# Kernel optimization log

Measured on AMD Instinct MI355X. Metric: run time of the kernel, lower is better.

Reference implementation:

```python
import jax, jax.numpy as jnp
from jax import lax
import numpy as np

B, H, W, D_MODEL = 2, 64, 64, 192
D_INNER, D_STATE, DT_RANK = 384, 16, 12
L = H * W
LN_EPS = 1e-5


def setup_inputs() -> dict:
    ks = jax.random.split(jax.random.key(0), 12)
    rng = np.random.default_rng(0)
    perm = rng.permutation(L).astype(np.int32)

    def p(i, shape, scale=0.02):
        return jax.random.normal(ks[i], shape, dtype=jnp.float32) * scale

    return {
        "x": jax.random.normal(ks[0], (B, H, W, D_MODEL), dtype=jnp.float32),
        "condition": jax.random.normal(ks[1], (B, H, W, D_MODEL), dtype=jnp.float32),
        "W_in": p(2, (2 * D_INNER, D_MODEL)),
        "W_con": p(3, (D_INNER, D_MODEL)),
        "conv_w": p(4, (D_INNER, 1, 3, 3)),
        "conv_b": jnp.zeros((D_INNER,), jnp.float32),
        "con_conv_w": p(5, (D_INNER, 1, 3, 3)),
        "con_conv_b": jnp.zeros((D_INNER,), jnp.float32),
        "x_proj_w": p(6, (DT_RANK + 2 * D_STATE, D_INNER)),
        "dt_proj_w": p(7, (D_INNER, DT_RANK)),
        "dt_proj_b": p(8, (D_INNER,), 0.1),
        "A_logs": jnp.tile(jnp.log(jnp.arange(1, D_STATE + 1, dtype=jnp.float32))[None, :], (D_INNER, 1)),
        "Ds": jnp.ones((D_INNER,), jnp.float32),
        "ln_w": jnp.ones((D_INNER,), jnp.float32),
        "ln_b": jnp.zeros((D_INNER,), jnp.float32),
        "W_out": p(9, (D_MODEL, D_INNER)),
        "scan_path": jnp.asarray(perm),
        "rev_scan_path": jnp.asarray(np.argsort(perm).astype(np.int32)),
    }


def _dwconv(x, w, b):
    # depthwise 3x3 conv, SAME padding; x: [B, C, H, W], w: [C, 1, 3, 3]
    y = lax.conv_general_dilated(x, w, (1, 1), "SAME",
                                 dimension_numbers=("NCHW", "OIHW", "NCHW"),
                                 feature_group_count=x.shape[1])
    return y + b[None, :, None, None]


def _selective_scan(u, delta, A, Bs, Cs, D):
    # u, delta: [B, D, L]; A: [D, N]; Bs, Cs: [B, N, L]; D: [D]
    dA = jnp.exp(jnp.einsum("bdl,dn->lbdn", delta, A))          # [L, B, D, N]
    dBu = jnp.einsum("bdl,bnl,bdl->lbdn", delta, Bs, u)          # [L, B, D, N]
    Ct = jnp.transpose(Cs, (2, 0, 1))                             # [L, B, N]
    h0 = jnp.zeros(dA.shape[1:], dA.dtype)

    def step(h, inp):
        a, b, c = inp
        h = a * h + b
        return h, jnp.einsum("bdn,bn->bd", h, c)

    _, ys = lax.scan(step, h0, (dA, dBu, Ct))                     # ys: [L, B, D]
    y = jnp.transpose(ys, (1, 2, 0))                              # [B, D, L]
    return y + u * D[None, :, None]


def _forward(x, condition, W_in, W_con, conv_w, conv_b, con_conv_w, con_conv_b,
             x_proj_w, dt_proj_w, dt_proj_b, A_logs, Ds, ln_w, ln_b, W_out,
             scan_path, rev_scan_path):
    b, h, w, _ = x.shape
    l = h * w
    xz = x @ W_in.T                                               # [B, H, W, 2*Din]
    xa, z = jnp.split(xz, 2, axis=-1)
    z = jax.nn.silu(z)
    c = condition @ W_con.T
    xa = jax.nn.silu(_dwconv(jnp.transpose(xa, (0, 3, 1, 2)), conv_w, conv_b))
    c = jax.nn.silu(_dwconv(jnp.transpose(c, (0, 3, 1, 2)), con_conv_w, con_conv_b))
    d = xa.shape[1]
    xs = xa.reshape(b, d, l)[:, :, scan_path]                     # forward_permutation, K=1
    cs = c.reshape(b, d, l)[:, :, scan_path]
    x_dbl = jnp.einsum("bdl,cd->bcl", xs + cs, x_proj_w)          # [B, R+2N, L]
    r, n = dt_proj_w.shape[1], A_logs.shape[1]
    dts = jnp.einsum("brl,dr->bdl", x_dbl[:, :r], dt_proj_w)
    Bs = x_dbl[:, r:r + n]
    Cs = x_dbl[:, r + n:]
    A = -jnp.exp(A_logs)
    delta = jax.nn.softplus(dts + dt_proj_b[None, :, None])       # delta_softplus=True
    y = _selective_scan(xs, delta, A, Bs, Cs, Ds)                 # [B, D, L]
    y = y[:, :, rev_scan_path]                                    # backward_permutation
    y = jnp.transpose(y, (0, 2, 1))                               # [B, L, D]
    mu = jnp.mean(y, axis=-1, keepdims=True)
    var = jnp.var(y, axis=-1, keepdims=True)
    y = (y - mu) * lax.rsqrt(var + LN_EPS) * ln_w + ln_b          # out_norm
    y = y.reshape(b, h, w, d) * z
    return y @ W_out.T                                            # out_proj (no bias)


def reference(x, condition, W_in, W_con, conv_w, conv_b, con_conv_w, con_conv_b,
              x_proj_w, dt_proj_w, dt_proj_b, A_logs, Ds, ln_w, ln_b, W_out,
              scan_path, rev_scan_path):
    return _forward(x, condition, W_in, W_con, conv_w, conv_b, con_conv_w,
                    con_conv_b, x_proj_w, dt_proj_w, dt_proj_b, A_logs, Ds,
                    ln_w, ln_b, W_out, scan_path, rev_scan_path)
```

## Files before the change

### kernel.cpp

```cpp
#include <hip/hip_runtime.h>
#include <math.h>

#define BB 2
#define HH 64
#define WW 64
#define DM 192
#define DI 384
#define NS 16
#define DTR 12
#define LL 4096
#define ROWS (BB*LL)
#define NCHUNK 64
#define LCHUNK 64
#define NCOMB 448

typedef __attribute__((ext_vector_type(8))) short bf16x8;
typedef __attribute__((ext_vector_type(4))) float f32x4;

__device__ __forceinline__ float silu_f(float v) {
    return v / (1.0f + __expf(-v));
}

__device__ __forceinline__ unsigned short f2bf(float f) {
    union { float f; unsigned int u; } c; c.f = f;
    unsigned int u = c.u;
    u += 0x7fffu + ((u >> 16) & 1u);
    return (unsigned short)(u >> 16);
}

__global__ __launch_bounds__(256) void cast_bf16(
    const float* __restrict__ in, unsigned short* __restrict__ out, int n4)
{
    int i = blockIdx.x * 256 + threadIdx.x;
    if (i >= n4) return;
    float4 v = ((const float4*)in)[i];
    ushort4 o;
    o.x = f2bf(v.x); o.y = f2bf(v.y); o.z = f2bf(v.z); o.w = f2bf(v.w);
    ((ushort4*)out)[i] = o;
}

__global__ __launch_bounds__(256) void cast_weights(
    const float* __restrict__ w_in, const float* __restrict__ w_con,
    const float* __restrict__ w_out,
    unsigned short* __restrict__ w_in_bf, unsigned short* __restrict__ w_con_bf,
    unsigned short* __restrict__ w_out_bf)
{
    int i = blockIdx.x * 256 + threadIdx.x;
    if (i >= 73728) return;
    const float4* src; ushort4* dst; int off;
    if (i < 36864)      { src = (const float4*)w_in;  dst = (ushort4*)w_in_bf;  off = i; }
    else if (i < 55296) { src = (const float4*)w_con; dst = (ushort4*)w_con_bf; off = i - 36864; }
    else                { src = (const float4*)w_out; dst = (ushort4*)w_out_bf; off = i - 55296; }
    float4 v = src[off];
    ushort4 o;
    o.x = f2bf(v.x); o.y = f2bf(v.y); o.z = f2bf(v.z); o.w = f2bf(v.w);
    dst[off] = o;
}

__global__ __launch_bounds__(256) void make_wcomb(
    const float* __restrict__ x_proj_w,
    const float* __restrict__ dt_w,
    unsigned short* __restrict__ wc)
{
    int idx = blockIdx.x * 256 + threadIdx.x;
    if (idx >= NCOMB * DI) return;
    int row = idx / DI, k = idx - row * DI;
    float v = 0.f;
    if (row < 384) {
        const float* dw = dt_w + row * DTR;
        #pragma unroll
        for (int r = 0; r < DTR; ++r) v += dw[r] * x_proj_w[r * DI + k];
    } else if (row < 416) {
        v = x_proj_w[(12 + (row - 384)) * DI + k];
    }
    wc[idx] = f2bf(v);
}

__device__ __forceinline__ void gemm_epilogue(
    int mode, int row, int col, int N, float v,
    const float* __restrict__ bias,
    float* __restrict__ out0, float* __restrict__ out1)
{
    if (mode == 0) {
        if (col < 384) out0[(size_t)row * 384 + col] = v;
        else           out1[(size_t)row * 384 + (col - 384)] = silu_f(v);
    } else if (mode == 1) {
        out0[(size_t)row * N + col] = v;
    } else {
        if (col < 384) {
            float a = v + bias[col];
            out0[(size_t)row * 384 + col] = (a > 20.f) ? a : log1pf(__expf(a));
        } else if (col < 416) {
            int idx = col - 384;
            int pos = (idx < 16) ? ((idx & 7) * 4 + (idx >> 3))
                                 : (((idx - 16) & 7) * 4 + 2 + ((idx - 16) >> 3));
            out1[(size_t)row * 32 + pos] = v;
        }
    }
}

__global__ __launch_bounds__(256) void gemm_bf16(
    const unsigned short* __restrict__ A, const unsigned short* __restrict__ W,
    const float* __restrict__ bias,
    float* __restrict__ out0, float* __restrict__ out1,
    int M, int N, int K, int mode)
{
    __shared__ __align__(16) unsigned short sA[64 * 40];
    __shared__ __align__(16) unsigned short sB[64 * 40];
    const int bm = blockIdx.x * 64;
    const int bn = blockIdx.y * 64;
    const int tid  = threadIdx.x;
    const int wave = tid >> 6;
    const int lane = tid & 63;
    const int quad = lane >> 4;
    const int l16  = lane & 15;

    const int lrow = tid >> 2;
    const int lkof = (tid & 3) * 8;

    f32x4 acc[4];
    #pragma unroll
    for (int t = 0; t < 4; ++t) acc[t] = (f32x4)(0.f);

    const int arow = (wave * 16 + l16) * 40 + quad * 8;

    for (int k0 = 0; k0 < K; k0 += 32) {
        *(bf16x8*)&sA[lrow * 40 + lkof] =
            *(const bf16x8*)&A[(size_t)(bm + lrow) * K + k0 + lkof];
        *(bf16x8*)&sB[lrow * 40 + lkof] =
            *(const bf16x8*)&W[(size_t)(bn + lrow) * K + k0 + lkof];
        __syncthreads();
        bf16x8 a = *(bf16x8*)&sA[arow];
        #pragma unroll
        for (int t = 0; t < 4; ++t) {
            bf16x8 b = *(bf16x8*)&sB[(t * 16 + l16) * 40 + quad * 8];
            acc[t] = __builtin_amdgcn_mfma_f32_16x16x32_bf16(a, b, acc[t], 0, 0, 0);
        }
        __syncthreads();
    }

    #pragma unroll
    for (int t = 0; t < 4; ++t) {
        int col = bn + t * 16 + l16;
        #pragma unroll
        for (int r = 0; r < 4; ++r) {
            int row = bm + wave * 16 + quad * 4 + r;
            gemm_epilogue(mode, row, col, N, acc[t][r], bias, out0, out1);
        }
    }
}

__global__ __launch_bounds__(256) void dwconv2_scatter(
    const float* __restrict__ xin, const float* __restrict__ cin,
    const float* __restrict__ wx, const float* __restrict__ bx,
    const float* __restrict__ wc, const float* __restrict__ bc,
    const int* __restrict__ rev_scan_path,
    float* __restrict__ xs_buf, unsigned short* __restrict__ s_bf)
{
    const int tile = blockIdx.x;
    const int c0   = blockIdx.y * 64;
    const int b    = blockIdx.z;
    const int h0 = (tile >> 3) * 8, w0 = (tile & 7) * 8;
    __shared__ float smx[10 * 10 * 64];
    __shared__ float smc[10 * 10 * 64];
    __shared__ int   jtile[64];

    for (int idx = threadIdx.x; idx < 6400; idx += 256) {
        int pix = idx >> 6, ch = idx & 63;
        int py = pix / 10, px = pix - py * 10;
        int gh = h0 + py - 1, gw = w0 + px - 1;
        float vx = 0.f, vc = 0.f;
        if (gh >= 0 && gh < 64 && gw >= 0 && gw < 64) {
            size_t g = ((size_t)(b * LL + gh * 64 + gw)) * DI + c0 + ch;
            vx = xin[g]; vc = cin[g];
        }
        smx[idx] = vx; smc[idx] = vc;
    }
    if (threadIdx.x < 64) {
        int l = (h0 + (threadIdx.x >> 3)) * 64 + (w0 + (threadIdx.x & 7));
        jtile[threadIdx.x] = rev_scan_path[l];
    }
    __syncthreads();

    const int ch = threadIdx.x & 63;
    const int pq = threadIdx.x >> 6;
    float wrx[9], wrc[9];
    #pragma unroll
    for (int k = 0; k < 9; ++k) {
        wrx[k] = wx[(c0 + ch) * 9 + k];
        wrc[k] = wc[(c0 + ch) * 9 + k];
    }
    const float bvx = bx[c0 + ch];
    const float bvc = bc[c0 + ch];

    #pragma unroll
    for (int i = 0; i < 16; ++i) {
        int p  = pq * 16 + i;
        int ph = p >> 3, pw = p & 7;
        float ax = bvx, ac = bvc;
        #pragma unroll
        for (int ki = 0; ki < 3; ++ki)
            #pragma unroll
            for (int kj = 0; kj < 3; ++kj) {
                int si = ((ph + ki) * 10 + (pw + kj)) * 64 + ch;
                ax += wrx[ki * 3 + kj] * smx[si];
                ac += wrc[ki * 3 + kj] * smc[si];
            }
        float xv = silu_f(ax);
        float sv = xv + silu_f(ac);
        size_t o = ((size_t)(b * LL + jtile[p])) * DI + c0 + ch;
        xs_buf[o] = xv;
        s_bf[o]   = f2bf(sv);
    }
}

__global__ __launch_bounds__(256) void scan_chunkA(
    const float* __restrict__ xs, const float* __restrict__ delta,
    const float* __restrict__ btct, const float* __restrict__ A_logs,
    float* __restrict__ chunkA, float* __restrict__ chunkB)
{
    const int c = blockIdx.x;
    const int g = blockIdx.y;
    const int b = blockIdx.z;
    const int t = threadIdx.x;
    const int grp = t >> 3, p = t & 7;
    const int d = g * 32 + grp;
    const float Av0 = -__expf(A_logs[d * NS + p]);
    const float Av1 = -__expf(A_logs[d * NS + p + 8]);
    const int j0 = c * LCHUNK;

    const float*  dl = delta + ((size_t)b * LL + j0) * DI + d;
    const float*  ul = xs    + ((size_t)b * LL + j0) * DI + d;
    const float2* bl = (const float2*)btct + ((size_t)b * LL + j0) * 16 + p * 2;

    float h0 = 0.f, h1 = 0.f, P0 = 1.f, P1 = 1.f;
    float dv[4], uv[4]; float2 bv[4];
    #pragma unroll
    for (int q = 0; q < 4; ++q) {
        dv[q] = dl[(size_t)q * DI]; uv[q] = ul[(size_t)q * DI]; bv[q] = bl[(size_t)q * 16];
    }
    for (int j = 0; j < LCHUNK; j += 4) {
        float nd[4], nu[4]; float2 nb[4];
        if (j + 4 < LCHUNK) {
            #pragma unroll
            for (int q = 0; q < 4; ++q) {
                int jj = j + 4 + q;
                nd[q] = dl[(size_t)jj * DI]; nu[q] = ul[(size_t)jj * DI]; nb[q] = bl[(size_t)jj * 16];
            }
        }
        #pragma unroll
        for (int q = 0; q < 4; ++q) {
            float e0 = __expf(dv[q] * Av0);
            float e1 = __expf(dv[q] * Av1);
            float du = dv[q] * uv[q];
            h0 = e0 * h0 + bv[q].x * du;
            h1 = e1 * h1 + bv[q].y * du;
            P0 *= e0; P1 *= e1;
        }
        #pragma unroll
        for (int q = 0; q < 4; ++q) { dv[q]=nd[q]; uv[q]=nu[q]; bv[q]=nb[q]; }
    }
    size_t idx = (((size_t)c * BB + b) * DI + d) * 8 + p;
    ((float2*)chunkA)[idx] = make_float2(P0, P1);
    ((float2*)chunkB)[idx] = make_float2(h0, h1);
}

__global__ __launch_bounds__(256) void scan_combine(
    const float* __restrict__ chunkA, const float* __restrict__ chunkB,
    float* __restrict__ hstart)
{
    const int gid = blockIdx.x * 256 + threadIdx.x;
    const size_t stride = (size_t)BB * DI * NS;
    float h = 0.f;
    float a = chunkA[gid], bv = chunkB[gid];
    for (int c = 0; c < NCHUNK; ++c) {
        float na = 0.f, nb = 0.f;
        if (c + 1 < NCHUNK) {
            na = chunkA[(size_t)(c + 1) * stride + gid];
            nb = chunkB[(size_t)(c + 1) * stride + gid];
        }
        hstart[(size_t)c * stride + gid] = h;
        h = a * h + bv;
        a = na; bv = nb;
    }
}

__global__ __launch_bounds__(256) void scan_chunkC(
    const float* __restrict__ xs, const float* __restrict__ delta,
    const float* __restrict__ btct,
    const float* __restrict__ A_logs, const float* __restrict__ Ds,
    const float* __restrict__ hstart,
    float* __restrict__ yt)
{
    const int c = blockIdx.x;
    const int g = blockIdx.y;
    const int b = blockIdx.z;
    const int t = threadIdx.x;
    const int grp = t >> 3, p = t & 7;
    const int d = g * 32 + grp;
    const float Av0 = -__expf(A_logs[d * NS + p]);
    const float Av1 = -__expf(A_logs[d * NS + p + 8]);
    const float Dv = Ds[d];
    const int j0 = c * LCHUNK;

    const float*  dl  = delta + ((size_t)b * LL + j0) * DI + d;
    const float*  ul  = xs    + ((size_t)b * LL + j0) * DI + d;
    const float4* bcl = (const float4*)btct + ((size_t)b * LL + j0) * 8 + p;
    float* yl = yt + ((size_t)b * LL + j0) * DI + d;

    float2 h = ((const float2*)hstart)[(((size_t)c * BB + b) * DI + d) * 8 + p];
    float h0 = h.x, h1 = h.y;

    float dv[4], uv[4]; float4 bc[4];
    #pragma unroll
    for (int q = 0; q < 4; ++q) {
        dv[q] = dl[(size_t)q * DI]; uv[q] = ul[(size_t)q * DI]; bc[q] = bcl[(size_t)q * 8];
    }
    for (int j = 0; j < LCHUNK; j += 4) {
        float nd[4], nu[4]; float4 nbc[4];
        if (j + 4 < LCHUNK) {
            #pragma unroll
            for (int q = 0; q < 4; ++q) {
                int jj = j + 4 + q;
                nd[q] = dl[(size_t)jj * DI]; nu[q] = ul[(size_t)jj * DI]; nbc[q] = bcl[(size_t)jj * 8];
            }
        }
        #pragma unroll
        for (int q = 0; q < 4; ++q) {
            float e0 = __expf(dv[q] * Av0);
            float e1 = __expf(dv[q] * Av1);
            float du = dv[q] * uv[q];
            h0 = e0 * h0 + bc[q].x * du;
            h1 = e1 * h1 + bc[q].y * du;
            float acc = h0 * bc[q].z + h1 * bc[q].w;
            acc += __shfl_xor(acc, 4, 8);
            acc += __shfl_xor(acc, 2, 8);
            acc += __shfl_xor(acc, 1, 8);
            if (p == 0) yl[(size_t)(j + q) * DI] = acc + uv[q] * Dv;
        }
        #pragma unroll
        for (int q = 0; q < 4; ++q) { dv[q]=nd[q]; uv[q]=nu[q]; bc[q]=nbc[q]; }
    }
}

__global__ __launch_bounds__(128) void ln_mul(
    const float* __restrict__ yt, const float* __restrict__ z,
    const int* __restrict__ scan_path,
    const float* __restrict__ ln_w, const float* __restrict__ ln_b,
    unsigned short* __restrict__ yn)
{
    const int j = blockIdx.x;
    const int b = blockIdx.y;
    const int l = scan_path[j];
    const int t = threadIdx.x;
    const float* row = yt + ((size_t)(b * LL + j)) * DI;
    float v0 = row[t], v1 = row[t + 128], v2 = row[t + 256];
    float s  = v0 + v1 + v2;
    float s2 = v0*v0 + v1*v1 + v2*v2;
    #pragma unroll
    for (int off = 32; off > 0; off >>= 1) {
        s  += __shfl_down(s, off);
        s2 += __shfl_down(s2, off);
    }
    __shared__ float red[4];
    if ((t & 63) == 0) { red[(t >> 6) * 2] = s; red[(t >> 6) * 2 + 1] = s2; }
    __syncthreads();
    float S  = red[0] + red[2];
    float S2 = red[1] + red[3];
    float mu  = S * (1.0f / DI);
    float var = S2 * (1.0f / DI) - mu * mu;
    float inv = rsqrtf(var + 1e-5f);

    const float* zr = z + ((size_t)(b * LL + l)) * DI;
    unsigned short* o = yn + ((size_t)(b * LL + l)) * DI;
    o[t]       = f2bf(((v0 - mu) * inv * ln_w[t]       + ln_b[t])       * zr[t]);
    o[t + 128] = f2bf(((v1 - mu) * inv * ln_w[t + 128] + ln_b[t + 128]) * zr[t + 128]);
    o[t + 256] = f2bf(((v2 - mu) * inv * ln_w[t + 256] + ln_b[t + 256]) * zr[t + 256]);
}

extern "C" void kernel_launch(void* const* d_in, const int* in_sizes, int n_in,
                              void* d_out, int out_size, void* d_ws, size_t ws_size,
                              hipStream_t stream) {
    const float* x          = (const float*)d_in[0];
    const float* cond       = (const float*)d_in[1];
    const float* W_in       = (const float*)d_in[2];
    const float* W_con      = (const float*)d_in[3];
    const float* conv_w     = (const float*)d_in[4];
    const float* conv_b     = (const float*)d_in[5];
    const float* con_conv_w = (const float*)d_in[6];
    const float* con_conv_b = (const float*)d_in[7];
    const float* x_proj_w   = (const float*)d_in[8];
    const float* dt_proj_w  = (const float*)d_in[9];
    const float* dt_proj_b  = (const float*)d_in[10];
    const float* A_logs     = (const float*)d_in[11];
    const float* Ds         = (const float*)d_in[12];
    const float* ln_w       = (const float*)d_in[13];
    const float* ln_b       = (const float*)d_in[14];
    const float* W_out      = (const float*)d_in[15];
    const int*   scan_path  = (const int*)d_in[16];
    const int*   rev_path   = (const int*)d_in[17];

    float* ws = (float*)d_ws;
    const size_t S  = (size_t)BB * LL * DI;
    const size_t SC = (size_t)NCHUNK * BB * DI * NS;
    float* xa_pre  = ws + 0 * S;
    float* z_silu  = ws + 1 * S;
    float* c_pre   = ws + 2 * S;
    float* xs_buf  = ws + 3 * S;
    float* dl_buf  = ws + 4 * S;
    float* btct    = ws + 5 * S;
    float* chunkA  = btct + (size_t)BB * LL * 32;
    float* chunkB  = chunkA + SC;
    float* hstart  = chunkB + SC;
    float* bfpool  = hstart + SC;

    unsigned short* x_bf    = (unsigned short*)bfpool;
    unsigned short* c_bf    = x_bf + (size_t)ROWS * DM;
    unsigned short* s_bf    = x_bf;
    unsigned short* w_in_bf  = c_bf + (size_t)ROWS * DM;
    unsigned short* w_con_bf = w_in_bf + 768 * DM;
    unsigned short* w_out_bf = w_con_bf + 384 * DM;
    unsigned short* wcomb_bf = w_out_bf + 192 * DI;
    unsigned short* yn_bf    = (unsigned short*)c_pre;
    float* yt = xa_pre;

    cast_bf16<<<(ROWS * DM / 4 + 255) / 256, 256, 0, stream>>>(x, x_bf, ROWS * DM / 4);
    cast_bf16<<<(ROWS * DM / 4 + 255) / 256, 256, 0, stream>>>(cond, c_bf, ROWS * DM / 4);
    cast_weights<<<(73728 + 255) / 256, 256, 0, stream>>>(
        W_in, W_con, W_out, w_in_bf, w_con_bf, w_out_bf);
    make_wcomb<<<(NCOMB * DI + 255) / 256, 256, 0, stream>>>(x_proj_w, dt_proj_w, wcomb_bf);

    gemm_bf16<<<dim3(ROWS / 64, 768 / 64), 256, 0, stream>>>(
        x_bf, w_in_bf, nullptr, xa_pre, z_silu, ROWS, 768, DM, 0);
    gemm_bf16<<<dim3(ROWS / 64, 384 / 64), 256, 0, stream>>>(
        c_bf, w_con_bf, nullptr, c_pre, nullptr, ROWS, 384, DM, 1);
    dwconv2_scatter<<<dim3(64, 6, BB), 256, 0, stream>>>(
        xa_pre, c_pre, conv_w, conv_b, con_conv_w, con_conv_b,
        rev_path, xs_buf, s_bf);
    gemm_bf16<<<dim3(ROWS / 64, NCOMB / 64), 256, 0, stream>>>(
        s_bf, wcomb_bf, dt_proj_b, dl_buf, btct, ROWS, NCOMB, DI, 2);
    scan_chunkA<<<dim3(NCHUNK, DI / 32, BB), 256, 0, stream>>>(
        xs_buf, dl_buf, btct, A_logs, chunkA, chunkB);
    scan_combine<<<(BB * DI * NS) / 256, 256, 0, stream>>>(chunkA, chunkB, hstart);
    scan_chunkC<<<dim3(NCHUNK, DI / 32, BB), 256, 0, stream>>>(
        xs_buf, dl_buf, btct, A_logs, Ds, hstart, yt);
    ln_mul<<<dim3(LL, BB), 128, 0, stream>>>(yt, z_silu, scan_path, ln_w, ln_b, yn_bf);
    gemm_bf16<<<dim3(ROWS / 64, 192 / 64), 256, 0, stream>>>(
        yn_bf, w_out_bf, nullptr, (float*)d_out, nullptr, ROWS, DM, DI, 1);
}
```

Before: 231.0 us.

## Fuse input bf16 cast into GEMM load and stage scan chunks in LDS

New measurement: 238.8 us. +3.3%, slower.

```diff
diff --git a/kernel.cpp b/kernel.cpp
--- a/kernel.cpp
+++ b/kernel.cpp
@@ -13,6 +13,7 @@
 #define NCHUNK 64
 #define LCHUNK 64
 #define NCOMB 448
+#define SROW 36
 
 typedef __attribute__((ext_vector_type(8))) short bf16x8;
 typedef __attribute__((ext_vector_type(4))) float f32x4;
@@ -28,15 +29,13 @@
     return (unsigned short)(u >> 16);
 }
 
-__global__ __launch_bounds__(256) void cast_bf16(
-    const float* __restrict__ in, unsigned short* __restrict__ out, int n4)
-{
-    int i = blockIdx.x * 256 + threadIdx.x;
-    if (i >= n4) return;
-    float4 v = ((const float4*)in)[i];
-    ushort4 o;
-    o.x = f2bf(v.x); o.y = f2bf(v.y); o.z = f2bf(v.z); o.w = f2bf(v.w);
-    ((ushort4*)out)[i] = o;
+__device__ __forceinline__ bf16x8 f2bf8(float4 a, float4 b) {
+    bf16x8 r;
+    r[0] = (short)f2bf(a.x); r[1] = (short)f2bf(a.y);
+    r[2] = (short)f2bf(a.z); r[3] = (short)f2bf(a.w);
+    r[4] = (short)f2bf(b.x); r[5] = (short)f2bf(b.y);
+    r[6] = (short)f2bf(b.z); r[7] = (short)f2bf(b.w);
+    return r;
 }
 
 __global__ __launch_bounds__(256) void cast_weights(
@@ -114,7 +113,6 @@
     const int lane = tid & 63;
     const int quad = lane >> 4;
     const int l16  = lane & 15;
-
     const int lrow = tid >> 2;
     const int lkof = (tid & 3) * 8;
 
@@ -127,6 +125,58 @@
     for (int k0 = 0; k0 < K; k0 += 32) {
         *(bf16x8*)&sA[lrow * 40 + lkof] =
             *(const bf16x8*)&A[(size_t)(bm + lrow) * K + k0 + lkof];
+        *(bf16x8*)&sB[lrow * 40 + lkof] =
+            *(const bf16x8*)&W[(size_t)(bn + lrow) * K + k0 + lkof];
+        __syncthreads();
+        bf16x8 a = *(bf16x8*)&sA[arow];
+        #pragma unroll
+        for (int t = 0; t < 4; ++t) {
+            bf16x8 b = *(bf16x8*)&sB[(t * 16 + l16) * 40 + quad * 8];
+            acc[t] = __builtin_amdgcn_mfma_f32_16x16x32_bf16(a, b, acc[t], 0, 0, 0);
+        }
+        __syncthreads();
+    }
+
+    #pragma unroll
+    for (int t = 0; t < 4; ++t) {
+        int col = bn + t * 16 + l16;
+        #pragma unroll
+        for (int r = 0; r < 4; ++r) {
+            int row = bm + wave * 16 + quad * 4 + r;
+            gemm_epilogue(mode, row, col, N, acc[t][r], bias, out0, out1);
+        }
+    }
+}
+
+__global__ __launch_bounds__(256) void gemm_bf16_f32a(
+    const float* __restrict__ A, const unsigned short* __restrict__ W,
+    const float* __restrict__ bias,
+    float* __restrict__ out0, float* __restrict__ out1,
+    int M, int N, int K, int mode)
+{
+    __shared__ __align__(16) unsigned short sA[64 * 40];
+    __shared__ __align__(16) unsigned short sB[64 * 40];
+    const int bm = blockIdx.x * 64;
+    const int bn = blockIdx.y * 64;
+    const int tid  = threadIdx.x;
+    const int wave = tid >> 6;
+    const int lane = tid & 63;
+    const int quad = lane >> 4;
+    const int l16  = lane & 15;
+    const int lrow = tid >> 2;
+    const int lkof = (tid & 3) * 8;
+
+    f32x4 acc[4];
+    #pragma unroll
+    for (int t = 0; t < 4; ++t) acc[t] = (f32x4)(0.f);
+
+    const int arow = (wave * 16 + l16) * 40 + quad * 8;
+
+    for (int k0 = 0; k0 < K; k0 += 32) {
+        const float* ap = &A[(size_t)(bm + lrow) * K + k0 + lkof];
+        float4 a0 = *(const float4*)ap;
+        float4 a1 = *(const float4*)(ap + 4);
+        *(bf16x8*)&sA[lrow * 40 + lkof] = f2bf8(a0, a1);
         *(bf16x8*)&sB[lrow * 40 + lkof] =
             *(const bf16x8*)&W[(size_t)(bn + lrow) * K + k0 + lkof];
         __syncthreads();
@@ -214,11 +264,31 @@
     }
 }
 
+__device__ __forceinline__ void stage_chunk(
+    const float* __restrict__ delta, const float* __restrict__ xs,
+    const float* __restrict__ btct, int b, int g, int j0, int t,
+    float* sD, float* sU, float* sBC)
+{
+    const int row0 = t >> 3;
+    const int c4   = t & 7;
+    #pragma unroll
+    for (int it = 0; it < 2; ++it) {
+        int row = row0 + it * 32;
+        size_t gr = ((size_t)(b * LL + j0 + row));
+        *(float4*)&sD[row * SROW + c4 * 4]  = *(const float4*)&delta[gr * DI + g * 32 + c4 * 4];
+        *(float4*)&sU[row * SROW + c4 * 4]  = *(const float4*)&xs[gr * DI + g * 32 + c4 * 4];
+        *(float4*)&sBC[row * SROW + c4 * 4] = *(const float4*)&btct[gr * 32 + c4 * 4];
+    }
+}
+
 __global__ __launch_bounds__(256) void scan_chunkA(
     const float* __restrict__ xs, const float* __restrict__ delta,
     const float* __restrict__ btct, const float* __restrict__ A_logs,
     float* __restrict__ chunkA, float* __restrict__ chunkB)
 {
+    __shared__ __align__(16) float sD[LCHUNK * SROW];
+    __shared__ __align__(16) float sU[LCHUNK * SROW];
+    __shared__ __align__(16) float sBC[LCHUNK * SROW];
     const int c = blockIdx.x;
     const int g = blockIdx.y;
     const int b = blockIdx.z;
@@ -229,39 +299,27 @@
     const float Av1 = -__expf(A_logs[d * NS + p + 8]);
     const int j0 = c * LCHUNK;
 
-    const float*  dl = delta + ((size_t)b * LL + j0) * DI + d;
-    const float*  ul = xs    + ((size_t)b * LL + j0) * DI + d;
-    const float2* bl = (const float2*)btct + ((size_t)b * LL + j0) * 16 + p * 2;
-
-    float h0 = 0.f, h1 = 0.f, P0 = 1.f, P1 = 1.f;
-    float dv[4], uv[4]; float2 bv[4];
-    #pragma unroll
-    for (int q = 0; q < 4; ++q) {
-        dv[q] = dl[(size_t)q * DI]; uv[q] = ul[(size_t)q * DI]; bv[q] = bl[(size_t)q * 16];
-    }
+    stage_chunk(delta, xs, btct, b, g, j0, t, sD, sU, sBC);
+    __syncthreads();
+
+    float h0 = 0.f, h1 = 0.f, Sdelta = 0.f;
     for (int j = 0; j < LCHUNK; j += 4) {
-        float nd[4], nu[4]; float2 nb[4];
-        if (j + 4 < LCHUNK) {
-            #pragma unroll
-            for (int q = 0; q < 4; ++q) {
-                int jj = j + 4 + q;
-                nd[q] = dl[(size_t)jj * DI]; nu[q] = ul[(size_t)jj * DI]; nb[q] = bl[(size_t)jj * 16];
-            }
-        }
         #pragma unroll
         for (int q = 0; q < 4; ++q) {
-            float e0 = __expf(dv[q] * Av0);
-            float e1 = __expf(dv[q] * Av1);
-            float du = dv[q] * uv[q];
-            h0 = e0 * h0 + bv[q].x * du;
-            h1 = e1 * h1 + bv[q].y * du;
-            P0 *= e0; P1 *= e1;
-        }
-        #pragma unroll
-        for (int q = 0; q < 4; ++q) { dv[q]=nd[q]; uv[q]=nu[q]; bv[q]=nb[q]; }
-    }
-    size_t idx = (((size_t)c * BB + b) * DI + d) * 8 + p;
-    ((float2*)chunkA)[idx] = make_float2(P0, P1);
+            int jj = j + q;
+            float dv = sD[jj * SROW + grp];
+            float uv = sU[jj * SROW + grp];
+            float2 bv = *(const float2*)&sBC[jj * SROW + p * 4];
+            float e0 = __expf(dv * Av0);
+            float e1 = __expf(dv * Av1);
+            float du = dv * uv;
+            h0 = e0 * h0 + bv.x * du;
+            h1 = e1 * h1 + bv.y * du;
+            Sdelta += dv;
+        }
+    }
+    size_t idx = (((size_t)b * DI + d) * 8 + p) * NCHUNK + c;
+    ((float2*)chunkA)[idx] = make_float2(__expf(Sdelta * Av0), __expf(Sdelta * Av1));
     ((float2*)chunkB)[idx] = make_float2(h0, h1);
 }
 
@@ -270,18 +328,15 @@
     float* __restrict__ hstart)
 {
     const int gid = blockIdx.x * 256 + threadIdx.x;
-    const size_t stride = (size_t)BB * DI * NS;
-    float h = 0.f;
-    float a = chunkA[gid], bv = chunkB[gid];
+    const float2* A2 = (const float2*)chunkA + (size_t)gid * NCHUNK;
+    const float2* B2 = (const float2*)chunkB + (size_t)gid * NCHUNK;
+    float2*       H2 = (float2*)hstart       + (size_t)gid * NCHUNK;
+    float h0 = 0.f, h1 = 0.f;
     for (int c = 0; c < NCHUNK; ++c) {
-        float na = 0.f, nb = 0.f;
-        if (c + 1 < NCHUNK) {
-            na = chunkA[(size_t)(c + 1) * stride + gid];
-            nb = chunkB[(size_t)(c + 1) * stride + gid];
-        }
-        hstart[(size_t)c * stride + gid] = h;
-        h = a * h + bv;
-        a = na; bv = nb;
+        float2 a = A2[c], bv = B2[c];
+        H2[c] = make_float2(h0, h1);
+        h0 = a.x * h0 + bv.x;
+        h1 = a.y * h1 + bv.y;
     }
 }
 
@@ -292,6 +347,9 @@
     const float* __restrict__ hstart,
     float* __restrict__ yt)
 {
+    __shared__ __align__(16) float sD[LCHUNK * SROW];
+    __shared__ __align__(16) float sU[LCHUNK * SROW];
+    __shared__ __align__(16) float sBC[LCHUNK * SROW];
     const int c = blockIdx.x;
     const int g = blockIdx.y;
     const int b = blockIdx.z;
@@ -303,43 +361,31 @@
     const float Dv = Ds[d];
     const int j0 = c * LCHUNK;
 
-    const float*  dl  = delta + ((size_t)b * LL + j0) * DI + d;
-    const float*  ul  = xs    + ((size_t)b * LL + j0) * DI + d;
-    const float4* bcl = (const float4*)btct + ((size_t)b * LL + j0) * 8 + p;
+    stage_chunk(delta, xs, btct, b, g, j0, t, sD, sU, sBC);
+
+    float2 h = ((const float2*)hstart)[(((size_t)b * DI + d) * 8 + p) * NCHUNK + c];
+    float h0 = h.x, h1 = h.y;
     float* yl = yt + ((size_t)b * LL + j0) * DI + d;
-
-    float2 h = ((const float2*)hstart)[(((size_t)c * BB + b) * DI + d) * 8 + p];
-    float h0 = h.x, h1 = h.y;
-
-    float dv[4], uv[4]; float4 bc[4];
-    #pragma unroll
-    for (int q = 0; q < 4; ++q) {
-        dv[q] = dl[(size_t)q * DI]; uv[q] = ul[(size_t)q * DI]; bc[q] = bcl[(size_t)q * 8];
-    }
+    __syncthreads();
+
     for (int j = 0; j < LCHUNK; j += 4) {
-        float nd[4], nu[4]; float4 nbc[4];
-        if (j + 4 < LCHUNK) {
-            #pragma unroll
-            for (int q = 0; q < 4; ++q) {
-                int jj = j + 4 + q;
-                nd[q] = dl[(size_t)jj * DI]; nu[q] = ul[(size_t)jj * DI]; nbc[q] = bcl[(size_t)jj * 8];
-            }
-        }
         #pragma unroll
         for (int q = 0; q < 4; ++q) {
-            float e0 = __expf(dv[q] * Av0);
-            float e1 = __expf(dv[q] * Av1);
-            float du = dv[q] * uv[q];
-            h0 = e0 * h0 + bc[q].x * du;
-            h1 = e1 * h1 + bc[q].y * du;
-            float acc = h0 * bc[q].z + h1 * bc[q].w;
+            int jj = j + q;
+            float dv = sD[jj * SROW + grp];
+            float uv = sU[jj * SROW + grp];
+            float4 bc = *(const float4*)&sBC[jj * SROW + p * 4];
+            float e0 = __expf(dv * Av0);
+            float e1 = __expf(dv * Av1);
+            float du = dv * uv;
+            h0 = e0 * h0 + bc.x * du;
+            h1 = e1 * h1 + bc.y * du;
+            float acc = h0 * bc.z + h1 * bc.w;
             acc += __shfl_xor(acc, 4, 8);
             acc += __shfl_xor(acc, 2, 8);
             acc += __shfl_xor(acc, 1, 8);
-            if (p == 0) yl[(size_t)(j + q) * DI] = acc + uv[q] * Dv;
-        }
-        #pragma unroll
-        for (int q = 0; q < 4; ++q) { dv[q]=nd[q]; uv[q]=nu[q]; bc[q]=nbc[q]; }
+            if (p == 0) yl[(size_t)jj * DI] = acc + uv * Dv;
+        }
     }
 }
 
@@ -414,26 +460,22 @@
     float* hstart  = chunkB + SC;
     float* bfpool  = hstart + SC;
 
-    unsigned short* x_bf    = (unsigned short*)bfpool;
-    unsigned short* c_bf    = x_bf + (size_t)ROWS * DM;
-    unsigned short* s_bf    = x_bf;
-    unsigned short* w_in_bf  = c_bf + (size_t)ROWS * DM;
+    unsigned short* s_bf     = (unsigned short*)bfpool;
+    unsigned short* w_in_bf  = s_bf + (size_t)ROWS * DI;
     unsigned short* w_con_bf = w_in_bf + 768 * DM;
     unsigned short* w_out_bf = w_con_bf + 384 * DM;
     unsigned short* wcomb_bf = w_out_bf + 192 * DI;
     unsigned short* yn_bf    = (unsigned short*)c_pre;
     float* yt = xa_pre;
 
-    cast_bf16<<<(ROWS * DM / 4 + 255) / 256, 256, 0, stream>>>(x, x_bf, ROWS * DM / 4);
-    cast_bf16<<<(ROWS * DM / 4 + 255) / 256, 256, 0, stream>>>(cond, c_bf, ROWS * DM / 4);
     cast_weights<<<(73728 + 255) / 256, 256, 0, stream>>>(
         W_in, W_con, W_out, w_in_bf, w_con_bf, w_out_bf);
     make_wcomb<<<(NCOMB * DI + 255) / 256, 256, 0, stream>>>(x_proj_w, dt_proj_w, wcomb_bf);
 
-    gemm_bf16<<<dim3(ROWS / 64, 768 / 64), 256, 0, stream>>>(
-        x_bf, w_in_bf, nullptr, xa_pre, z_silu, ROWS, 768, DM, 0);
-    gemm_bf16<<<dim3(ROWS / 64, 384 / 64), 256, 0, stream>>>(
-        c_bf, w_con_bf, nullptr, c_pre, nullptr, ROWS, 384, DM, 1);
+    gemm_bf16_f32a<<<dim3(ROWS / 64, 768 / 64), 256, 0, stream>>>(
+        x, w_in_bf, nullptr, xa_pre, z_silu, ROWS, 768, DM, 0);
+    gemm_bf16_f32a<<<dim3(ROWS / 64, 384 / 64), 256, 0, stream>>>(
+        cond, w_con_bf, nullptr, c_pre, nullptr, ROWS, 384, DM, 1);
     dwconv2_scatter<<<dim3(64, 6, BB), 256, 0, stream>>>(
         xa_pre, c_pre, conv_w, conv_b, con_conv_w, con_conv_b,
         rev_path, xs_buf, s_bf);
@@ -441,7 +483,7 @@
         s_bf, wcomb_bf, dt_proj_b, dl_buf, btct, ROWS, NCOMB, DI, 2);
     scan_chunkA<<<dim3(NCHUNK, DI / 32, BB), 256, 0, stream>>>(
         xs_buf, dl_buf, btct, A_logs, chunkA, chunkB);
-    scan_combine<<<(BB * DI * NS) / 256, 256, 0, stream>>>(chunkA, chunkB, hstart);
+    scan_combine<<<(BB * DI * 8) / 256, 256, 0, stream>>>(chunkA, chunkB, hstart);
     scan_chunkC<<<dim3(NCHUNK, DI / 32, BB), 256, 0, stream>>>(
         xs_buf, dl_buf, btct, A_logs, Ds, hstart, yt);
     ln_mul<<<dim3(LL, BB), 128, 0, stream>>>(yt, z_silu, scan_path, ln_w, ln_b, yn_bf);
```
